# Kernel optimization log

Measured on AMD Instinct MI355X. Metric: run time of the kernel, lower is better.

## Reference

```python
import jax, jax.numpy as jnp
import numpy as np

N = 100_000      # nodes
E = 1_600_000    # nonzeros of the rescaled Laplacian (avg degree 16)
F_IN = 128
F_OUT = 128
K = 4


def setup_inputs() -> dict:
    key = jax.random.key(0)
    ks = jax.random.split(key, 6)
    x = jax.random.normal(ks[0], (N, F_IN), dtype=jnp.float32)
    filter_coeff = jax.random.normal(ks[1], (K, N), dtype=jnp.float32)
    # glorot-ish scale for [K, F_in, F_out]
    stdv = float(np.sqrt(6.0 / (F_IN + F_OUT)))
    weight = jax.random.uniform(ks[2], (K, F_IN, F_OUT), dtype=jnp.float32,
                                minval=-stdv, maxval=stdv)
    bias = jnp.zeros((F_OUT,), dtype=jnp.float32)
    src = jax.random.randint(ks[3], (E,), 0, N, dtype=jnp.int32)
    dst = jax.random.randint(ks[4], (E,), 0, N, dtype=jnp.int32)
    # edge values of L_hat = 2L/lambda_max - I (precomputed sparse matrix)
    edge_w = jax.random.normal(ks[5], (E,), dtype=jnp.float32) * 0.1
    return {"x": x, "filter_coeff": filter_coeff, "weight": weight,
            "bias": bias, "edge_w": edge_w, "src": src, "dst": dst}


def reference(x, filter_coeff, weight, bias, edge_w, src, dst):
    n = x.shape[0]

    def spmm(h):  # edge-weighted gather-scale-segment_sum == dgl.update_all
        return jax.ops.segment_sum(h[src] * edge_w[:, None], dst,
                                   num_segments=n)

    # Chebyshev recurrence: T0 = x, T1 = L_hat x, T_k = 2 L_hat T_{k-1} - T_{k-2}
    Tx0 = x
    out = (filter_coeff[0][:, None] * Tx0) @ weight[0]
    Tx1 = spmm(x)
    out = out + (filter_coeff[1][:, None] * Tx1) @ weight[1]
    for k in range(2, weight.shape[0]):
        Tx2 = 2.0 * spmm(Tx1) - Tx0
        out = out + (filter_coeff[k][:, None] * Tx2) @ weight[k]
        Tx0, Tx1 = Tx1, Tx2
    return out + bias
```

## Files before the change

kernel.cpp:

```cpp
#include <hip/hip_runtime.h>
#include <hip/hip_bf16.h>
#include <cstdio>

#define F 128
#define BSHIFT 9
#define BROWS 512
#define C2 4096

typedef __attribute__((ext_vector_type(4))) float f32x4;
typedef __attribute__((ext_vector_type(4))) unsigned short u16x4;
typedef __attribute__((ext_vector_type(8))) short s16x8;

__device__ inline unsigned short f2bf(float x) {
  unsigned int u = __float_as_uint(x);
  u += 0x7fffu + ((u >> 16) & 1u);
  return (unsigned short)(u >> 16);
}
__device__ inline float bf2f(unsigned int h) {
  return __uint_as_float(h << 16);
}

__device__ inline void async_load16(const void* g, void* l) {
  __builtin_amdgcn_global_load_lds(
      (const __attribute__((address_space(1))) void*)g,
      (__attribute__((address_space(3))) void*)l, 16, 0, 0);
}

__global__ void bucket_hist_kernel(const int* __restrict__ dst, int* __restrict__ bhist,
                                   int E, int B) {
  __shared__ int h[256];
  int t = threadIdx.x;
  h[t] = 0;
  __syncthreads();
  for (int e = blockIdx.x * blockDim.x + t; e < E; e += gridDim.x * blockDim.x)
    atomicAdd(&h[dst[e] >> BSHIFT], 1);
  __syncthreads();
  if (t < B && h[t]) atomicAdd(&bhist[t], h[t]);
}

__global__ void bucket_scan_kernel(const int* __restrict__ bhist, int* __restrict__ bbase,
                                   int* __restrict__ bcursor, int* __restrict__ rp,
                                   int E, int B, int N) {
  __shared__ int sm[256];
  int t = threadIdx.x;
  int v = (t < B) ? bhist[t] : 0;
  sm[t] = v;
  __syncthreads();
  int x = v;
  for (int off = 1; off < 256; off <<= 1) {
    int add = (t >= off) ? sm[t - off] : 0;
    __syncthreads();
    x += add;
    sm[t] = x;
    __syncthreads();
  }
  int excl = x - v;
  if (t < B) { bbase[t] = excl; bcursor[t] = excl; }
  if (t == 0) { bbase[B] = E; rp[N] = E; }
}

__global__ __launch_bounds__(256) void bucket_scatter_kernel(
    const int* __restrict__ src, const int* __restrict__ dst, const float* __restrict__ ew,
    int* __restrict__ bcursor, unsigned int* __restrict__ stg_p, float* __restrict__ stg_w,
    int E, int B) {
  __shared__ int hist[256], gbase[256], cur[256], sm[256], scn[256];
  __shared__ unsigned int sp[C2];
  __shared__ float swt[C2];
  __shared__ int sdest[C2];
  int t = threadIdx.x;
  int e0 = blockIdx.x * C2;
  int cnt = min(C2, E - e0);
  hist[t] = 0;
  __syncthreads();
#pragma unroll
  for (int i = 0; i < C2 / 256; ++i) {
    int e = e0 + t + i * 256;
    if (e < E) atomicAdd(&hist[dst[e] >> BSHIFT], 1);
  }
  __syncthreads();
  int v = hist[t];
  gbase[t] = (t < B && v) ? atomicAdd(&bcursor[t], v) : 0;
  sm[t] = v;
  __syncthreads();
  int x = v;
  for (int off = 1; off < 256; off <<= 1) {
    int add = (t >= off) ? sm[t - off] : 0;
    __syncthreads();
    x += add;
    sm[t] = x;
    __syncthreads();
  }
  scn[t] = x - v;
  cur[t] = 0;
  __syncthreads();
#pragma unroll
  for (int i = 0; i < C2 / 256; ++i) {
    int e = e0 + t + i * 256;
    if (e < E) {
      int d = dst[e];
      int b = d >> BSHIFT;
      int r = atomicAdd(&cur[b], 1);
      int slot = scn[b] + r;
      sp[slot] = (unsigned int)src[e] | ((unsigned int)(d & (BROWS - 1)) << 17);
      swt[slot] = ew[e];
      sdest[slot] = gbase[b] + r;
    }
  }
  __syncthreads();
#pragma unroll
  for (int i = 0; i < C2 / 256; ++i) {
    int s = t + i * 256;
    if (s < cnt) {
      int dpos = sdest[s];
      stg_p[dpos] = sp[s];
      stg_w[dpos] = swt[s];
    }
  }
}

__global__ __launch_bounds__(256) void csr_build_kernel(
    const unsigned int* __restrict__ stg_p, const float* __restrict__ stg_w,
    const int* __restrict__ bbase, int* __restrict__ rp, int2* __restrict__ csr,
    int N, int B) {
  __shared__ int rhist[BROWS], rloc[BROWS], curp[BROWS];
  __shared__ int sm[256];
  int b = blockIdx.x, t = threadIdx.x;
  int row0 = b << BSHIFT;
  int base = bbase[b];
  int cnt = bbase[b + 1] - base;
  rhist[t] = 0;
  rhist[t + 256] = 0;
  __syncthreads();
  for (int s = base + t; s < base + cnt; s += 256)
    atomicAdd(&rhist[stg_p[s] >> 17], 1);
  __syncthreads();
  int a0 = rhist[2 * t], a1 = rhist[2 * t + 1];
  int pv = a0 + a1;
  sm[t] = pv;
  __syncthreads();
  int x = pv;
  for (int off = 1; off < 256; off <<= 1) {
    int add = (t >= off) ? sm[t - off] : 0;
    __syncthreads();
    x += add;
    sm[t] = x;
    __syncthreads();
  }
  int pexcl = x - pv;
  int r0 = 2 * t, r1 = 2 * t + 1;
  rloc[r0] = pexcl;
  rloc[r1] = pexcl + a0;
  if (row0 + r0 < N) rp[row0 + r0] = base + rloc[r0];
  if (row0 + r1 < N) rp[row0 + r1] = base + rloc[r1];
  curp[r0] = base + rloc[r0];
  curp[r1] = base + rloc[r1];
  __syncthreads();
  for (int s = base + t; s < base + cnt; s += 256) {
    unsigned int p = stg_p[s];
    int dl = p >> 17;
    int pos = atomicAdd(&curp[dl], 1);
    int2 entry;
    entry.x = (int)(p & 0x1ffffu);
    entry.y = __float_as_int(stg_w[s]);
    csr[pos] = entry;
  }
}

__global__ void convx_kernel(const float* __restrict__ x, unsigned short* __restrict__ xbf,
                             int total4) {
  int i = blockIdx.x * 256 + threadIdx.x;
  if (i >= total4) return;
  f32x4 v = ((const f32x4*)x)[i];
  u16x4 o;
  o.x = f2bf(v.x); o.y = f2bf(v.y); o.z = f2bf(v.z); o.w = f2bf(v.w);
  ((u16x4*)xbf)[i] = o;
}

__global__ __launch_bounds__(256) void spmm_kernel(
    const unsigned short* __restrict__ Tin, const unsigned short* __restrict__ Tsub,
    unsigned short* __restrict__ Tout, const int* __restrict__ rp,
    const int2* __restrict__ csr, int n, float scale) {
  int row = blockIdx.x * 16 + (threadIdx.x >> 4);
  if (row >= n) return;
  int sl = threadIdx.x & 15;
  int j0 = rp[row], end = rp[row + 1];
  const uint4* Tin4 = (const uint4*)Tin;
  float acc[8];
#pragma unroll
  for (int c = 0; c < 8; ++c) acc[c] = 0.f;

  for (int j = j0; j < end; j += 8) {
    int2 e[8];
#pragma unroll
    for (int u = 0; u < 8; ++u)
      if (j + u < end) e[u] = csr[j + u];
    uint4 v[8];
#pragma unroll
    for (int u = 0; u < 8; ++u)
      if (j + u < end) v[u] = Tin4[(size_t)e[u].x * 16 + sl];
#pragma unroll
    for (int u = 0; u < 8; ++u) {
      if (j + u < end) {
        float w = __int_as_float(e[u].y);
        acc[0] = fmaf(w, bf2f(v[u].x & 0xffffu), acc[0]);
        acc[1] = fmaf(w, bf2f(v[u].x >> 16), acc[1]);
        acc[2] = fmaf(w, bf2f(v[u].y & 0xffffu), acc[2]);
        acc[3] = fmaf(w, bf2f(v[u].y >> 16), acc[3]);
        acc[4] = fmaf(w, bf2f(v[u].z & 0xffffu), acc[4]);
        acc[5] = fmaf(w, bf2f(v[u].z >> 16), acc[5]);
        acc[6] = fmaf(w, bf2f(v[u].w & 0xffffu), acc[6]);
        acc[7] = fmaf(w, bf2f(v[u].w >> 16), acc[7]);
      }
    }
  }

  float r[8];
#pragma unroll
  for (int c = 0; c < 8; ++c) r[c] = scale * acc[c];
  if (Tsub) {
    uint4 p = ((const uint4*)Tsub)[(size_t)row * 16 + sl];
    r[0] -= bf2f(p.x & 0xffffu); r[1] -= bf2f(p.x >> 16);
    r[2] -= bf2f(p.y & 0xffffu); r[3] -= bf2f(p.y >> 16);
    r[4] -= bf2f(p.z & 0xffffu); r[5] -= bf2f(p.z >> 16);
    r[6] -= bf2f(p.w & 0xffffu); r[7] -= bf2f(p.w >> 16);
  }
  uint4 o;
  o.x = (unsigned)f2bf(r[0]) | ((unsigned)f2bf(r[1]) << 16);
  o.y = (unsigned)f2bf(r[2]) | ((unsigned)f2bf(r[3]) << 16);
  o.z = (unsigned)f2bf(r[4]) | ((unsigned)f2bf(r[5]) << 16);
  o.w = (unsigned)f2bf(r[6]) | ((unsigned)f2bf(r[7]) << 16);
  ((uint4*)Tout)[(size_t)row * 16 + sl] = o;
}

__global__ void convw_kernel(const float* __restrict__ W, unsigned short* __restrict__ Wf,
                             int total) {
  int idx = blockIdx.x * 256 + threadIdx.x;
  if (idx >= total) return;
  int j = idx & 7;
  int lane = (idx >> 3) & 63;
  int nt = (idx >> 9) & 7;
  int kk = (idx >> 12) & 3;
  int ks = idx >> 14;
  int kl = kk * 32 + (lane >> 4) * 8 + j;
  int col = nt * 16 + (lane & 15);
  Wf[idx] = f2bf(W[(size_t)ks * F * F + (size_t)kl * F + col]);
}

struct GemmArgs {
  const unsigned short* A[8];
  const float* fc;
  const unsigned short* Wt;
  const float* bias;
  float* out;
  int n;
  int kslices;
};

__global__ __launch_bounds__(256, 4) void gemm_kernel(GemmArgs args) {
  __shared__ __align__(16) unsigned short SB[16384];
  const int t = threadIdx.x;
  const int lane = t & 63;
  const int wid = t >> 6;
  const int wrow = wid >> 1, wcol = wid & 1;
  const int n = args.n;
  const int r0 = blockIdx.x * 64 + wrow * 32;
  const int arow = lane & 15;
  const int kg = lane >> 4;
  const bool live = r0 < n;

  f32x4 Cf[2][4];
#pragma unroll
  for (int mt = 0; mt < 2; ++mt)
#pragma unroll
    for (int nt = 0; nt < 4; ++nt) Cf[mt][nt] = (f32x4){0.f, 0.f, 0.f, 0.f};

  int row_a[2];
#pragma unroll
  for (int mt = 0; mt < 2; ++mt) {
    int r = r0 + mt * 16 + arow;
    row_a[mt] = (live && r < n) ? r : 0;
    if (live && r >= n) row_a[mt] = n - 1;
  }

  for (int ks = 0; ks < args.kslices; ++ks) {
#pragma unroll
    for (int i = 0; i < 8; ++i) {
      int chunk = wid * 8 + i;
      const void* g = (const void*)(args.Wt + (size_t)ks * 16384 + chunk * 512 + lane * 8);
      void* l = (void*)(SB + chunk * 512);
      async_load16(g, l);
    }
    __syncthreads();

    if (live) {
      const unsigned short* As = args.A[ks];
      f32x4 acc[2][4];
#pragma unroll
      for (int mt = 0; mt < 2; ++mt)
#pragma unroll
        for (int nt = 0; nt < 4; ++nt) acc[mt][nt] = (f32x4){0.f, 0.f, 0.f, 0.f};

#pragma unroll
      for (int kk = 0; kk < 4; ++kk) {
        s16x8 af[2], bfr[4];
#pragma unroll
        for (int mt = 0; mt < 2; ++mt)
          af[mt] = *(const s16x8*)(As + (size_t)row_a[mt] * F + kk * 32 + kg * 8);
#pragma unroll
        for (int nt = 0; nt < 4; ++nt)
          bfr[nt] = *(const s16x8*)&SB[(kk * 8 + wcol * 4 + nt) * 512 + lane * 8];
#pragma unroll
        for (int mt = 0; mt < 2; ++mt)
#pragma unroll
          for (int nt = 0; nt < 4; ++nt)
            acc[mt][nt] = __builtin_amdgcn_mfma_f32_16x16x32_bf16(af[mt], bfr[nt],
                                                                  acc[mt][nt], 0, 0, 0);
      }

#pragma unroll
      for (int mt = 0; mt < 2; ++mt) {
        int row = r0 + mt * 16 + kg * 4;
        f32x4 fv;
        if (row + 3 < n) {
          fv = *(const f32x4*)(args.fc + (size_t)ks * n + row);
        } else {
#pragma unroll
          for (int r4 = 0; r4 < 4; ++r4) {
            int rr = row + r4;
            if (rr >= n) rr = n - 1;
            fv[r4] = args.fc[(size_t)ks * n + rr];
          }
        }
#pragma unroll
        for (int nt = 0; nt < 4; ++nt) Cf[mt][nt] += fv * acc[mt][nt];
      }
    }
    __syncthreads();
  }

  if (!live) return;
#pragma unroll
  for (int nt = 0; nt < 4; ++nt) {
    int col = (wcol * 4 + nt) * 16 + arow;
    float bv = args.bias[col];
#pragma unroll
    for (int mt = 0; mt < 2; ++mt) {
#pragma unroll
      for (int r4 = 0; r4 < 4; ++r4) {
        int row = r0 + mt * 16 + kg * 4 + r4;
        if (row < n) args.out[(size_t)row * F + col] = Cf[mt][nt][r4] + bv;
      }
    }
  }
}

extern "C" void kernel_launch(void* const* d_in, const int* in_sizes, int n_in,
                              void* d_out, int out_size, void* d_ws, size_t ws_size,
                              hipStream_t stream) {
  const float* x    = (const float*)d_in[0];
  const float* fc   = (const float*)d_in[1];
  const float* W    = (const float*)d_in[2];
  const float* bias = (const float*)d_in[3];
  const float* ew   = (const float*)d_in[4];
  const int*   src  = (const int*)d_in[5];
  const int*   dst  = (const int*)d_in[6];

  const int N = in_sizes[0] / F;
  const int K = in_sizes[2] / (F * F);
  const int E = in_sizes[4];
  const int B = (N + BROWS - 1) >> BSHIFT;

  size_t off = 0;
  char* base = (char*)d_ws;
  auto alloc = [&](size_t bytes) -> void* {
    void* p = base + off;
    off += (bytes + 511) & ~(size_t)511;
    return p;
  };
  int* rp              = (int*)alloc(((size_t)N + 1) * 4);
  int* bhist           = (int*)alloc(1024);
  int* bbase           = (int*)alloc(1040);
  int* bcursor         = (int*)alloc(1024);
  int2* csr            = (int2*)alloc((size_t)E * 8);
  unsigned short* Wt   = (unsigned short*)alloc((size_t)K * F * F * 2);
  unsigned short* xbf  = (unsigned short*)alloc((size_t)N * F * 2);
  unsigned short* T[8];
  T[0] = xbf;
  for (int k = 1; k < K && k < 8; ++k) T[k] = (unsigned short*)alloc((size_t)N * F * 2);
  unsigned int* stg_p;
  float* stg_w;
  if (K >= 3 && (size_t)N * F * 2 >= (size_t)E * 8) {
    stg_p = (unsigned int*)T[2];
    stg_w = (float*)(T[2] + (size_t)E * 2);
  } else {
    stg_p = (unsigned int*)alloc((size_t)E * 4);
    stg_w = (float*)alloc((size_t)E * 4);
  }
  if (off > ws_size) {
    fprintf(stderr, "kernel_launch: ws too small: need %zu have %zu\n", off, ws_size);
    return;
  }

  hipMemsetAsync(bhist, 0, 1024, stream);
  int hblocks = (E + 255) / 256;
  if (hblocks > 2048) hblocks = 2048;
  hipLaunchKernelGGL(bucket_hist_kernel, dim3(hblocks), dim3(256), 0, stream, dst, bhist, E, B);
  hipLaunchKernelGGL(bucket_scan_kernel, dim3(1), dim3(256), 0, stream, bhist, bbase, bcursor,
                     rp, E, B, N);
  int sblocks = (E + C2 - 1) / C2;
  hipLaunchKernelGGL(bucket_scatter_kernel, dim3(sblocks), dim3(256), 0, stream, src, dst, ew,
                     bcursor, stg_p, stg_w, E, B);
  hipLaunchKernelGGL(csr_build_kernel, dim3(B), dim3(256), 0, stream, stg_p, stg_w, bbase,
                     rp, csr, N, B);

  int total4 = N * F / 4;
  hipLaunchKernelGGL(convx_kernel, dim3((total4 + 255) / 256), dim3(256), 0, stream,
                     x, xbf, total4);

  int sb = (N + 15) / 16;
  if (K > 1)
    hipLaunchKernelGGL(spmm_kernel, dim3(sb), dim3(256), 0, stream, xbf,
                       (const unsigned short*)nullptr, T[1], rp, csr, N, 1.0f);
  for (int k = 2; k < K; ++k) {
    const unsigned short* prev = T[k - 2];
    hipLaunchKernelGGL(spmm_kernel, dim3(sb), dim3(256), 0, stream, T[k - 1], prev, T[k],
                       rp, csr, N, 2.0f);
  }

  int total = K * F * F;
  hipLaunchKernelGGL(convw_kernel, dim3((total + 255) / 256), dim3(256), 0, stream, W, Wt,
                     total);

  GemmArgs ga;
  for (int k = 0; k < 8; ++k) ga.A[k] = (k < K) ? T[k] : xbf;
  ga.fc = fc; ga.Wt = Wt; ga.bias = bias;
  ga.out = (float*)d_out;
  ga.n = N; ga.kslices = K;
  hipLaunchKernelGGL(gemm_kernel, dim3((N + 63) / 64), dim3(256), 0, stream, ga);
}
```

Measured before the change: 359.2 us.

## Stage A tiles in LDS via async loads and enlarge GEMM block to 128 rows

After: 369.6 us. 1.03x slower.

```diff
diff --git a/kernel.cpp b/kernel.cpp
--- a/kernel.cpp
+++ b/kernel.cpp
@@ -256,17 +256,18 @@
   int kslices;
 };
 
-__global__ __launch_bounds__(256, 4) void gemm_kernel(GemmArgs args) {
+__global__ __launch_bounds__(512) void gemm_kernel(GemmArgs args) {
+  __shared__ __align__(16) unsigned short SA[16384];
   __shared__ __align__(16) unsigned short SB[16384];
   const int t = threadIdx.x;
   const int lane = t & 63;
   const int wid = t >> 6;
-  const int wrow = wid >> 1, wcol = wid & 1;
+  const int wrow = wid >> 1;
+  const int wcol = wid & 1;
   const int n = args.n;
-  const int r0 = blockIdx.x * 64 + wrow * 32;
+  const int bm = blockIdx.x * 128;
   const int arow = lane & 15;
   const int kg = lane >> 4;
-  const bool live = r0 < n;
 
   f32x4 Cf[2][4];
 #pragma unroll
@@ -274,71 +275,70 @@
 #pragma unroll
     for (int nt = 0; nt < 4; ++nt) Cf[mt][nt] = (f32x4){0.f, 0.f, 0.f, 0.f};
 
-  int row_a[2];
-#pragma unroll
-  for (int mt = 0; mt < 2; ++mt) {
-    int r = r0 + mt * 16 + arow;
-    row_a[mt] = (live && r < n) ? r : 0;
-    if (live && r >= n) row_a[mt] = n - 1;
-  }
-
   for (int ks = 0; ks < args.kslices; ++ks) {
-#pragma unroll
-    for (int i = 0; i < 8; ++i) {
-      int chunk = wid * 8 + i;
-      const void* g = (const void*)(args.Wt + (size_t)ks * 16384 + chunk * 512 + lane * 8);
-      void* l = (void*)(SB + chunk * 512);
-      async_load16(g, l);
-    }
-    __syncthreads();
-
-    if (live) {
-      const unsigned short* As = args.A[ks];
-      f32x4 acc[2][4];
+    const unsigned short* As = args.A[ks];
+#pragma unroll
+    for (int i = 0; i < 4; ++i) {
+      int fi = wid + i * 8;
+      int rg = fi >> 2, kk = fi & 3;
+      int r = bm + rg * 16 + arow;
+      if (r >= n) r = n - 1;
+      const void* g = (const void*)(As + (size_t)r * F + kk * 32 + kg * 8);
+      async_load16(g, (void*)(SA + fi * 512));
+    }
+#pragma unroll
+    for (int i = 0; i < 4; ++i) {
+      int fi = wid + i * 8;
+      const void* g = (const void*)(args.Wt + (size_t)ks * 16384 + fi * 512 + lane * 8);
+      async_load16(g, (void*)(SB + fi * 512));
+    }
+    __syncthreads();
+
+    f32x4 acc[2][4];
+#pragma unroll
+    for (int mt = 0; mt < 2; ++mt)
+#pragma unroll
+      for (int nt = 0; nt < 4; ++nt) acc[mt][nt] = (f32x4){0.f, 0.f, 0.f, 0.f};
+
+#pragma unroll
+    for (int kk = 0; kk < 4; ++kk) {
+      s16x8 af[2], bfr[4];
+#pragma unroll
+      for (int mt = 0; mt < 2; ++mt) {
+        int rg = wrow * 2 + mt;
+        af[mt] = *(const s16x8*)&SA[(rg * 4 + kk) * 512 + lane * 8];
+      }
+#pragma unroll
+      for (int nt = 0; nt < 4; ++nt)
+        bfr[nt] = *(const s16x8*)&SB[(kk * 8 + wcol * 4 + nt) * 512 + lane * 8];
 #pragma unroll
       for (int mt = 0; mt < 2; ++mt)
 #pragma unroll
-        for (int nt = 0; nt < 4; ++nt) acc[mt][nt] = (f32x4){0.f, 0.f, 0.f, 0.f};
-
-#pragma unroll
-      for (int kk = 0; kk < 4; ++kk) {
-        s16x8 af[2], bfr[4];
-#pragma unroll
-        for (int mt = 0; mt < 2; ++mt)
-          af[mt] = *(const s16x8*)(As + (size_t)row_a[mt] * F + kk * 32 + kg * 8);
-#pragma unroll
         for (int nt = 0; nt < 4; ++nt)
-          bfr[nt] = *(const s16x8*)&SB[(kk * 8 + wcol * 4 + nt) * 512 + lane * 8];
-#pragma unroll
-        for (int mt = 0; mt < 2; ++mt)
-#pragma unroll
-          for (int nt = 0; nt < 4; ++nt)
-            acc[mt][nt] = __builtin_amdgcn_mfma_f32_16x16x32_bf16(af[mt], bfr[nt],
-                                                                  acc[mt][nt], 0, 0, 0);
+          acc[mt][nt] = __builtin_amdgcn_mfma_f32_16x16x32_bf16(af[mt], bfr[nt],
+                                                                acc[mt][nt], 0, 0, 0);
+    }
+
+#pragma unroll
+    for (int mt = 0; mt < 2; ++mt) {
+      int row = bm + wrow * 32 + mt * 16 + kg * 4;
+      f32x4 fv;
+      if (row + 3 < n) {
+        fv = *(const f32x4*)(args.fc + (size_t)ks * n + row);
+      } else {
+#pragma unroll
+        for (int r4 = 0; r4 < 4; ++r4) {
+          int rr = row + r4;
+          if (rr >= n) rr = n - 1;
+          fv[r4] = args.fc[(size_t)ks * n + rr];
+        }
       }
-
-#pragma unroll
-      for (int mt = 0; mt < 2; ++mt) {
-        int row = r0 + mt * 16 + kg * 4;
-        f32x4 fv;
-        if (row + 3 < n) {
-          fv = *(const f32x4*)(args.fc + (size_t)ks * n + row);
-        } else {
-#pragma unroll
-          for (int r4 = 0; r4 < 4; ++r4) {
-            int rr = row + r4;
-            if (rr >= n) rr = n - 1;
-            fv[r4] = args.fc[(size_t)ks * n + rr];
-          }
-        }
-#pragma unroll
-        for (int nt = 0; nt < 4; ++nt) Cf[mt][nt] += fv * acc[mt][nt];
-      }
-    }
-    __syncthreads();
-  }
-
-  if (!live) return;
+#pragma unroll
+      for (int nt = 0; nt < 4; ++nt) Cf[mt][nt] += fv * acc[mt][nt];
+    }
+    __syncthreads();
+  }
+
 #pragma unroll
   for (int nt = 0; nt < 4; ++nt) {
     int col = (wcol * 4 + nt) * 16 + arow;
@@ -347,7 +347,7 @@
     for (int mt = 0; mt < 2; ++mt) {
 #pragma unroll
       for (int r4 = 0; r4 < 4; ++r4) {
-        int row = r0 + mt * 16 + kg * 4 + r4;
+        int row = bm + wrow * 32 + mt * 16 + kg * 4 + r4;
         if (row < n) args.out[(size_t)row * F + col] = Cf[mt][nt][r4] + bv;
       }
     }
@@ -436,5 +436,5 @@
   ga.fc = fc; ga.Wt = Wt; ga.bias = bias;
   ga.out = (float*)d_out;
   ga.n = N; ga.kslices = K;
-  hipLaunchKernelGGL(gemm_kernel, dim3((N + 63) / 64), dim3(256), 0, stream, ga);
-}
+  hipLaunchKernelGGL(gemm_kernel, dim3((N + 127) / 128), dim3(512), 0, stream, ga);
+}
```
